# Performance work log

Hardware: AMD Instinct MI355X
Metric: run time of the kernel (lower is better)

The kernel has to match this reference:

```python
import jax, jax.numpy as jnp
import numpy as np
from jax import lax

P = 16        # patch spatial size (C = 3 * P * P = 768)
CH = 3        # channels per patch
H = 8         # num attention heads
EPS_BN = 1e-3 # keras BatchNormalization default epsilon
EPS_LN = 1e-3 # keras LayerNormalization default epsilon


def _layernorm(x, g, b):
    mu = jnp.mean(x, axis=-1, keepdims=True)
    var = jnp.mean(jnp.square(x - mu), axis=-1, keepdims=True)
    return (x - mu) * lax.rsqrt(var + EPS_LN) * g + b


def setup_inputs() -> dict:
    key = jax.random.key(0)
    ks = jax.random.split(key, 8)
    B, N, C, DFF = 8, 1024, 768, 3072
    s = 0.02
    return {
        "encoded_patches": jax.random.normal(ks[0], (B, N, C), jnp.float32),
        "qconv_w": jax.random.normal(ks[1], (3, 3, CH, CH), jnp.float32) * 0.2,
        "reatten_w": jax.random.normal(ks[2], (H, H), jnp.float32) * 0.3,
        "reatten_b": jnp.zeros((H,), jnp.float32),
        "bn_gamma": jnp.ones((H,), jnp.float32),
        "bn_beta": jnp.zeros((H,), jnp.float32),
        "proj_w": jax.random.normal(ks[3], (C, C), jnp.float32) * s,
        "proj_b": jnp.zeros((C,), jnp.float32),
        "ffn_w1": jax.random.normal(ks[4], (C, DFF), jnp.float32) * s,
        "ffn_b1": jnp.zeros((DFF,), jnp.float32),
        "ffn_w2": jax.random.normal(ks[5], (DFF, C), jnp.float32) * s,
        "ffn_b2": jnp.zeros((C,), jnp.float32),
        "ln1_g": jnp.ones((C,), jnp.float32),
        "ln1_b": jnp.zeros((C,), jnp.float32),
        "ln2_g": jnp.ones((C,), jnp.float32),
        "ln2_b": jnp.zeros((C,), jnp.float32),
    }


def reference(encoded_patches, qconv_w, reatten_w, reatten_b, bn_gamma, bn_beta,
              proj_w, proj_b, ffn_w1, ffn_b1, ffn_w2, ffn_b2,
              ln1_g, ln1_b, ln2_g, ln2_b):
    B, N, C = encoded_patches.shape
    hd = C // H
    scale = jnp.float32(hd) ** -0.5

    # create_queries: unflatten [B,N,C] -> [B*N,P,P,CH], 3x3 'same' conv,
    # flatten back and split heads -> [B,H,N,hd]. Source uses qconv2d for
    # q, k AND v, so q == k == v; compute once.
    y = encoded_patches.reshape(B * N, P, P, CH)
    y = lax.conv_general_dilated(y, qconv_w, (1, 1), 'SAME',
                                 dimension_numbers=('NHWC', 'HWIO', 'NHWC'))
    q = y.reshape(B, N, H, hd).transpose(0, 2, 1, 3)  # [B,H,N,hd]
    k = q
    v = q

    # attention scores + softmax: [B,H,N,N]
    attn = jax.nn.softmax(jnp.einsum('bhnd,bhmd->bhnm', q, k) * scale, axis=-1)

    # re-attention: 1x1 conv mixing heads + BatchNorm (inference: mean=0, var=1)
    attn = jnp.einsum('bhnm,gh->bgnm', attn, reatten_w) + reatten_b[None, :, None, None]
    bn_s = bn_gamma * lax.rsqrt(jnp.float32(1.0) + EPS_BN)
    attn = attn * bn_s[None, :, None, None] + bn_beta[None, :, None, None]
    # reatten_scale = 1.0 (transform_scale=False)

    x = jnp.einsum('bhnm,bhmd->bhnd', attn, v)        # [B,H,N,hd]
    x = x.transpose(0, 2, 1, 3).reshape(B, N, C)
    x = x @ proj_w + proj_b

    x = x + encoded_patches          # residual
    x = _layernorm(x, ln1_g, ln1_b)  # LN1

    h = jax.nn.gelu(x @ ffn_w1 + ffn_b1, approximate=False)
    x = (h @ ffn_w2 + ffn_b2) + x    # FFN + residual
    x = _layernorm(x, ln2_g, ln2_b)  # LN2
    return x
```

## Files before the change

### kernel.cpp

```cpp
#include <hip/hip_runtime.h>
#include <hip/hip_bf16.h>
#include <math.h>

#define B_ 8
#define N_ 1024
#define C_ 768
#define H_ 8
#define HD_ 96
#define DFF_ 3072
#define SC2_ 0.14724454f
#define SH2_ 11.5415602f

typedef __attribute__((ext_vector_type(8))) short bf16x8;
typedef __attribute__((ext_vector_type(4))) float f32x4;
typedef __attribute__((ext_vector_type(4))) short sh4;

__device__ __forceinline__ short f2bf(float f){
  __hip_bfloat16 h = __float2bfloat16(f);
  return __builtin_bit_cast(short, h);
}
__device__ __forceinline__ float bf2f(short s){
  unsigned u = ((unsigned)(unsigned short)s) << 16;
  return __builtin_bit_cast(float, u);
}
#define MFMA16(a,b,c) __builtin_amdgcn_mfma_f32_16x16x32_bf16((a),(b),(c),0,0,0)

__device__ __forceinline__ void gload16(const void* g, void* l){
  __builtin_amdgcn_global_load_lds((const __attribute__((address_space(1))) unsigned int*)g,
                                   (__attribute__((address_space(3))) unsigned int*)l, 16, 0, 0);
}

__global__ void conv_q_kernel(const float* __restrict__ x, const float* __restrict__ w,
                              short* __restrict__ qb){
  int p = blockIdx.x;
  int t = threadIdx.x;
  __shared__ float xs[768];
  __shared__ float ws[81];
  const float* xp = x + (size_t)p * 768;
  xs[t] = xp[t]; xs[t+256] = xp[t+256]; xs[t+512] = xp[t+512];
  if (t < 81) ws[t] = w[t];
  __syncthreads();
  int i = t >> 4, j = t & 15;
  float a0=0.f, a1=0.f, a2=0.f;
  #pragma unroll
  for (int di=0; di<3; ++di){
    int ii = i + di - 1;
    if (ii < 0 || ii > 15) continue;
    #pragma unroll
    for (int dj=0; dj<3; ++dj){
      int jj = j + dj - 1;
      if (jj < 0 || jj > 15) continue;
      const float* cell = &xs[(ii*16+jj)*3];
      const float* wp = &ws[(di*3+dj)*9];
      #pragma unroll
      for (int ci=0; ci<3; ++ci){
        float xv = cell[ci];
        a0 += xv * wp[ci*3+0];
        a1 += xv * wp[ci*3+1];
        a2 += xv * wp[ci*3+2];
      }
    }
  }
  short* qp = qb + (size_t)p*768 + t*3;
  qp[0]=f2bf(a0); qp[1]=f2bf(a1); qp[2]=f2bf(a2);
}

__global__ void vt_kernel(const short* __restrict__ in, short* __restrict__ out){
  __shared__ short tile[32][33];
  int b = blockIdx.z;
  int c0 = blockIdx.x*32, n0 = blockIdx.y*32;
  int t = threadIdx.x;
  const short* ib = in + (size_t)b*N_*C_;
  short* ob = out + (size_t)b*C_*N_;
  #pragma unroll
  for (int i=0;i<4;i++){
    int idx = i*256+t; int r = idx>>5, cc = idx&31;
    tile[r][cc] = ib[(size_t)(n0+r)*C_ + c0+cc];
  }
  __syncthreads();
  #pragma unroll
  for (int i=0;i<4;i++){
    int idx = i*256+t; int r = idx>>5, cc = idx&31;
    ob[(size_t)(c0+r)*N_ + n0+cc] = tile[cc][r];
  }
}

__global__ void wtrans_kernel(const float* __restrict__ in, short* __restrict__ out,
                              int K, int Nn){
  __shared__ float tile[32][33];
  int n0 = blockIdx.x*32, k0 = blockIdx.y*32;
  int t = threadIdx.x;
  #pragma unroll
  for (int i=0;i<4;i++){
    int idx=i*256+t; int r=idx>>5, cc=idx&31;
    tile[r][cc] = in[(size_t)(k0+r)*Nn + n0+cc];
  }
  __syncthreads();
  #pragma unroll
  for (int i=0;i<4;i++){
    int idx=i*256+t; int r=idx>>5, cc=idx&31;
    out[(size_t)(n0+r)*K + k0+cc] = f2bf(tile[cc][r]);
  }
}

__global__ __launch_bounds__(256, 2)
void qkexp_kernel(const short* __restrict__ qb, short* __restrict__ Pt,
                  float* __restrict__ lsums, int b0)
{
  __shared__ short Ks[64*104];
  int bid = blockIdx.x;
  int bhl = bid >> 4, nt = bid & 15;
  int b = b0 + (bhl >> 3), h = bhl & 7;
  int n0 = nt*64;
  int t = threadIdx.x, w = t>>6, l = t&63, lg = l>>4, lr = l&15;
  const short* qbase = qb + (size_t)b*N_*C_;

  bf16x8 qf[3];
  #pragma unroll
  for (int kc=0;kc<3;++kc)
    qf[kc] = *(const bf16x8*)(qbase + (size_t)(n0 + w*16 + lr)*C_ + h*HD_ + kc*32 + lg*8);

  bf16x8 kreg[3];
  #pragma unroll
  for (int i=0;i<3;++i){
    int id = i*256+t; int r = id/12, c = id%12;
    kreg[i] = *(const bf16x8*)(qbase + (size_t)r*C_ + h*HD_ + c*8);
  }

  float lsum = 0.f;
  short* prow = Pt + ((size_t)bhl*1024 + n0 + w*16 + lr)*1024;

  for (int mt=0; mt<16; ++mt){
    int m0 = mt*64;
    __syncthreads();
    #pragma unroll
    for (int i=0;i<3;++i){
      int id = i*256+t; int r = id/12, c = id%12;
      *(bf16x8*)&Ks[r*104 + c*8] = kreg[i];
    }
    __syncthreads();
    if (mt < 15){
      int m1 = m0 + 64;
      #pragma unroll
      for (int i=0;i<3;++i){
        int id = i*256+t; int r = id/12, c = id%12;
        kreg[i] = *(const bf16x8*)(qbase + (size_t)(m1+r)*C_ + h*HD_ + c*8);
      }
    }
    #pragma unroll
    for (int s=0;s<4;++s){
      f32x4 sacc = (f32x4){0.f,0.f,0.f,0.f};
      bf16x8 kf[3];
      #pragma unroll
      for (int kc=0;kc<3;++kc)
        kf[kc] = *(const bf16x8*)&Ks[(s*16+lr)*104 + kc*32 + lg*8];
      #pragma unroll
      for (int kc=0;kc<3;++kc)
        sacc = MFMA16(kf[kc], qf[kc], sacc);
      sh4 pv;
      #pragma unroll
      for (int r=0;r<4;++r){
        float e = exp2f(sacc[r]*SC2_ - SH2_);
        lsum += e;
        pv[r] = f2bf(e);
      }
      *(sh4*)&prow[m0 + s*16 + lg*4] = pv;
    }
  }
  lsum += __shfl_xor(lsum, 16);
  lsum += __shfl_xor(lsum, 32);
  if (l < 16) lsums[(size_t)bhl*1024 + n0 + w*16 + l] = lsum;
}

__device__ __forceinline__ void load_mix(const short* __restrict__ Pt, int b_local,
                                         int n0, int m0, int t,
                                         const float wl[4][8], float cw, bf16x8 amc[4]){
  #pragma unroll
  for (int i=0;i<4;++i){
    int r = i*32 + (t>>3), mo = t&7;
    const short* p0 = Pt + ((size_t)(b_local*8)*1024 + (size_t)(n0+r))*1024 + m0 + mo*8;
    float pm[8];
    #pragma unroll
    for (int j=0;j<8;++j) pm[j] = cw;
    #pragma unroll
    for (int h=0;h<8;++h){
      bf16x8 ph = *(const bf16x8*)(p0 + (size_t)h*1024*1024);
      #pragma unroll
      for (int j=0;j<8;++j) pm[j] += wl[i][h]*bf2f(ph[j]);
    }
    #pragma unroll
    for (int j=0;j<8;++j) amc[i][j] = f2bf(pm[j]);
  }
}

__global__ __launch_bounds__(256, 2)
void mixpv_kernel(const short* __restrict__ Pt, const float* __restrict__ lsums,
                  const short* __restrict__ vt, const float* __restrict__ rw,
                  const float* __restrict__ rb, const float* __restrict__ bng,
                  const float* __restrict__ bnb, short* __restrict__ out, int b0)
{
  __shared__ short Am[128*68];
  int bid = blockIdx.x;
  int rank = bid>>3;
  int g = rank & 7;
  int p = (bid&7) + ((rank>>3)<<3);
  int b_local = p>>3;
  int n0 = (p&7)*128;
  int b = b0 + b_local;
  int t = threadIdx.x, w = t>>6, l = t&63, lg = l>>4, lr = l&15;

  float bns = bng[g]*rsqrtf(1.001f);
  float cw = rb[g]*bns + bnb[g];
  float wl[4][8];
  #pragma unroll
  for (int i=0;i<4;++i){
    int r = i*32 + (t>>3);
    #pragma unroll
    for (int h=0;h<8;++h)
      wl[i][h] = (rw[g*8+h]*bns) / lsums[(size_t)(b_local*8+h)*1024 + n0 + r];
  }

  f32x4 acc[2][6];
  #pragma unroll
  for (int a=0;a<2;++a)
    #pragma unroll
    for (int nt=0;nt<6;++nt) acc[a][nt] = (f32x4){0.f,0.f,0.f,0.f};

  bf16x8 amc[4];
  load_mix(Pt, b_local, n0, 0, t, wl, cw, amc);
  const short* vbase = vt + (size_t)b*C_*N_ + (size_t)g*HD_*N_;

  for (int mt=0; mt<16; ++mt){
    int m0 = mt*64;
    __syncthreads();
    #pragma unroll
    for (int i=0;i<4;++i){
      int r = i*32 + (t>>3), mo = t&7;
      *(bf16x8*)&Am[r*68 + mo*8] = amc[i];
    }
    __syncthreads();
    if (mt < 15) load_mix(Pt, b_local, n0, m0+64, t, wl, cw, amc);
    #pragma unroll
    for (int kc=0;kc<2;++kc){
      bf16x8 af[2], bfr[6];
      #pragma unroll
      for (int a=0;a<2;++a)
        af[a] = *(const bf16x8*)&Am[(w*32 + a*16 + lr)*68 + kc*32 + lg*8];
      #pragma unroll
      for (int nt=0;nt<6;++nt)
        bfr[nt] = *(const bf16x8*)(vbase + (size_t)(nt*16+lr)*N_ + m0 + kc*32 + lg*8);
      #pragma unroll
      for (int a=0;a<2;++a)
        #pragma unroll
        for (int nt=0;nt<6;++nt)
          acc[a][nt] = MFMA16(af[a], bfr[nt], acc[a][nt]);
    }
  }

  short* obase = out + (size_t)b*N_*C_;
  #pragma unroll
  for (int a=0;a<2;++a)
    #pragma unroll
    for (int nt=0;nt<6;++nt)
      #pragma unroll
      for (int r=0;r<4;++r)
        obase[(size_t)(n0 + w*32 + a*16 + lg*4 + r)*C_ + g*HD_ + nt*16 + lr]
            = f2bf(acc[a][nt][r]);
}

template<int EPI>
__global__ __launch_bounds__(256, 3)
void gemm_bt_kernel(const short* __restrict__ A, const short* __restrict__ Bt,
                    const float* __restrict__ bias, const float* __restrict__ res,
                    float* __restrict__ Of, short* __restrict__ Ob,
                    int M, int Nn, int K)
{
  __shared__ short As[8192];
  __shared__ short Bs[8192];
  int gm = blockIdx.y*128, gn = blockIdx.x*128;
  int tid = threadIdx.x;
  int w = tid>>6, l = tid&63, lg = l>>4, lr = l&15;
  int wr = w>>1, wc = w&1;
  f32x4 acc[4][4];
  #pragma unroll
  for (int mt=0;mt<4;++mt)
    #pragma unroll
    for (int nt=0;nt<4;++nt) acc[mt][nt] = (f32x4){0.f,0.f,0.f,0.f};

  int srow = l>>3, scol = (l&7)*8;

  for (int kb=0; kb<K; kb+=64){
    __syncthreads();
    #pragma unroll
    for (int j=0;j<4;++j){
      int row = j*32 + w*8 + srow;
      gload16(A  + (size_t)(gm+row)*K + kb + scol, &As[j*2048 + w*512]);
      gload16(Bt + (size_t)(gn+row)*K + kb + scol, &Bs[j*2048 + w*512]);
    }
    __syncthreads();
    #pragma unroll
    for (int kc=0;kc<2;++kc){
      bf16x8 af[4], bfr[4];
      #pragma unroll
      for (int mt=0;mt<4;++mt)
        af[mt] = *(const bf16x8*)&As[(wr*64+mt*16+lr)*64 + kc*32 + lg*8];
      #pragma unroll
      for (int nt=0;nt<4;++nt)
        bfr[nt] = *(const bf16x8*)&Bs[(wc*64+nt*16+lr)*64 + kc*32 + lg*8];
      #pragma unroll
      for (int mt=0;mt<4;++mt)
        #pragma unroll
        for (int nt=0;nt<4;++nt)
          acc[mt][nt] = MFMA16(af[mt], bfr[nt], acc[mt][nt]);
    }
  }
  #pragma unroll
  for (int mt=0;mt<4;++mt){
    #pragma unroll
    for (int nt=0;nt<4;++nt){
      #pragma unroll
      for (int r=0;r<4;++r){
        int row = gm + wr*64 + mt*16 + lg*4 + r;
        int col = gn + wc*64 + nt*16 + lr;
        float v = acc[mt][nt][r] + bias[col];
        if (EPI == 0){
          v += res[(size_t)row*Nn + col];
          Of[(size_t)row*Nn + col] = v;
        } else {
          v = 0.5f*v*(1.0f + erff(v*0.70710678118654752f));
          Ob[(size_t)row*Nn + col] = f2bf(v);
        }
      }
    }
  }
}

template<int WB>
__global__ void ln_kernel(const float* __restrict__ in, const float* __restrict__ gam,
                          const float* __restrict__ bet, float* __restrict__ of,
                          short* __restrict__ ob)
{
  int row = blockIdx.x*4 + (threadIdx.x>>6);
  int l = threadIdx.x & 63;
  const float* ip = in + (size_t)row*C_;
  float v[12];
  #pragma unroll
  for (int i=0;i<3;i++) *(float4*)&v[i*4] = *(const float4*)(ip + i*256 + l*4);
  float s = 0.f;
  #pragma unroll
  for (int i=0;i<12;i++) s += v[i];
  #pragma unroll
  for (int off=1; off<64; off<<=1) s += __shfl_xor(s, off);
  float mu = s * (1.0f/768.0f);
  float q = 0.f;
  #pragma unroll
  for (int i=0;i<12;i++){ float d = v[i]-mu; q += d*d; }
  #pragma unroll
  for (int off=1; off<64; off<<=1) q += __shfl_xor(q, off);
  float rstd = rsqrtf(q*(1.0f/768.0f) + 1e-3f);
  #pragma unroll
  for (int i=0;i<3;i++){
    float4 gv = *(const float4*)(gam + i*256 + l*4);
    float4 bv = *(const float4*)(bet + i*256 + l*4);
    float o0 = (v[i*4+0]-mu)*rstd*gv.x + bv.x;
    float o1 = (v[i*4+1]-mu)*rstd*gv.y + bv.y;
    float o2 = (v[i*4+2]-mu)*rstd*gv.z + bv.z;
    float o3 = (v[i*4+3]-mu)*rstd*gv.w + bv.w;
    float4 ov = {o0,o1,o2,o3};
    *(float4*)(of + (size_t)row*C_ + i*256 + l*4) = ov;
    if (WB){
      sh4 obv = { f2bf(o0), f2bf(o1), f2bf(o2), f2bf(o3) };
      *(sh4*)(ob + (size_t)row*C_ + i*256 + l*4) = obv;
    }
  }
}

extern "C" void kernel_launch(void* const* d_in, const int* in_sizes, int n_in,
                              void* d_out, int out_size, void* d_ws, size_t ws_size,
                              hipStream_t stream)
{
  const float* enc       = (const float*)d_in[0];
  const float* qconv_w   = (const float*)d_in[1];
  const float* reatten_w = (const float*)d_in[2];
  const float* reatten_b = (const float*)d_in[3];
  const float* bn_gamma  = (const float*)d_in[4];
  const float* bn_beta   = (const float*)d_in[5];
  const float* proj_w    = (const float*)d_in[6];
  const float* proj_b    = (const float*)d_in[7];
  const float* ffn_w1    = (const float*)d_in[8];
  const float* ffn_b1    = (const float*)d_in[9];
  const float* ffn_w2    = (const float*)d_in[10];
  const float* ffn_b2    = (const float*)d_in[11];
  const float* ln1_g     = (const float*)d_in[12];
  const float* ln1_b     = (const float*)d_in[13];
  const float* ln2_g     = (const float*)d_in[14];
  const float* ln2_b     = (const float*)d_in[15];
  float* outp = (float*)d_out;

  char* ws = (char*)d_ws;
  short* qbuf  = (short*)(ws);
  short* vtbuf = (short*)(ws + 12582912);
  short* atbuf = (short*)(ws + 25165824);
  short* ptbuf = (short*)(ws + 37748736);
  float* lsums = (float*)(ws + 104857600);
  float* ypre  = (float*)(ws + 37748736);
  float* x1    = (float*)(ws + 62914560);
  short* x1b   = (short*)(ws + 88080384);
  short* hbuf  = (short*)(ws + 100663296);
  short* wpt   = (short*)(ws + 150994944);
  short* w1t   = (short*)(ws + 152174592);
  short* w2t   = (short*)(ws + 156893184);

  conv_q_kernel<<<B_*N_, 256, 0, stream>>>(enc, qconv_w, qbuf);
  vt_kernel<<<dim3(C_/32, N_/32, B_), 256, 0, stream>>>(qbuf, vtbuf);
  wtrans_kernel<<<dim3(C_/32,  C_/32), 256, 0, stream>>>(proj_w, wpt, C_,  C_);
  wtrans_kernel<<<dim3(DFF_/32, C_/32), 256, 0, stream>>>(ffn_w1, w1t, C_,  DFF_);
  wtrans_kernel<<<dim3(C_/32, DFF_/32), 256, 0, stream>>>(ffn_w2, w2t, DFF_, C_);

  for (int half=0; half<2; ++half){
    int b0 = half*4;
    qkexp_kernel<<<512, 256, 0, stream>>>(qbuf, ptbuf, lsums, b0);
    mixpv_kernel<<<256, 256, 0, stream>>>(ptbuf, lsums, vtbuf, reatten_w, reatten_b,
                                          bn_gamma, bn_beta, atbuf, b0);
  }

  gemm_bt_kernel<0><<<dim3(C_/128, (B_*N_)/128), 256, 0, stream>>>(
      atbuf, wpt, proj_b, enc, ypre, nullptr, B_*N_, C_, C_);
  ln_kernel<1><<<(B_*N_)/4, 256, 0, stream>>>(ypre, ln1_g, ln1_b, x1, x1b);
  gemm_bt_kernel<1><<<dim3(DFF_/128, (B_*N_)/128), 256, 0, stream>>>(
      x1b, w1t, ffn_b1, nullptr, nullptr, hbuf, B_*N_, DFF_, C_);
  gemm_bt_kernel<0><<<dim3(C_/128, (B_*N_)/128), 256, 0, stream>>>(
      hbuf, w2t, ffn_b2, x1, ypre, nullptr, B_*N_, C_, DFF_);
  ln_kernel<0><<<(B_*N_)/4, 256, 0, stream>>>(ypre, ln2_g, ln2_b, outp, nullptr);
}
```

Baseline: 404.0 us.

## Double-buffer GEMM LDS tiles with XOR swizzle and stage epilogue through LDS

The bf16 GEMM kernel now double-buffers its A/B tiles in a 64KB LDS region, so the next K-slab loads while MFMAs run on the current one. LDS reads and writes use an XOR swizzle to avoid bank conflicts. The epilogue writes accumulators to LDS and then does coalesced float4 reads of bias and residual and vectorized stores, instead of scattered scalar accesses. The larger LDS footprint lowers the occupancy target from 3 to 2 blocks per CU.

```diff
diff --git a/kernel.cpp b/kernel.cpp
--- a/kernel.cpp
+++ b/kernel.cpp
@@ -269,68 +269,113 @@
 }
 
 template<int EPI>
-__global__ __launch_bounds__(256, 3)
+__global__ __launch_bounds__(256, 2)
 void gemm_bt_kernel(const short* __restrict__ A, const short* __restrict__ Bt,
                     const float* __restrict__ bias, const float* __restrict__ res,
                     float* __restrict__ Of, short* __restrict__ Ob,
                     int M, int Nn, int K)
 {
-  __shared__ short As[8192];
-  __shared__ short Bs[8192];
+  __shared__ __align__(16) char smem[65536];
+  short* Sb = (short*)smem;
   int gm = blockIdx.y*128, gn = blockIdx.x*128;
   int tid = threadIdx.x;
   int w = tid>>6, l = tid&63, lg = l>>4, lr = l&15;
   int wr = w>>1, wc = w&1;
+  int srow = l>>3;
+  int sg = (l&7) ^ srow;
+
+  const short* Ap = A  + (size_t)(gm + w*8 + srow)*K + sg*8;
+  const short* Bp = Bt + (size_t)(gn + w*8 + srow)*K + sg*8;
+
   f32x4 acc[4][4];
   #pragma unroll
   for (int mt=0;mt<4;++mt)
     #pragma unroll
     for (int nt=0;nt<4;++nt) acc[mt][nt] = (f32x4){0.f,0.f,0.f,0.f};
 
-  int srow = l>>3, scol = (l&7)*8;
-
-  for (int kb=0; kb<K; kb+=64){
-    __syncthreads();
+  int nk = K >> 6;
+
+  {
+    short* dA = Sb; short* dB = Sb + 8192;
     #pragma unroll
     for (int j=0;j<4;++j){
-      int row = j*32 + w*8 + srow;
-      gload16(A  + (size_t)(gm+row)*K + kb + scol, &As[j*2048 + w*512]);
-      gload16(Bt + (size_t)(gn+row)*K + kb + scol, &Bs[j*2048 + w*512]);
-    }
-    __syncthreads();
+      gload16(Ap + (size_t)j*32*K, dA + (j*32 + w*8)*64);
+      gload16(Bp + (size_t)j*32*K, dB + (j*32 + w*8)*64);
+    }
+  }
+  asm volatile("s_waitcnt vmcnt(0)" ::: "memory");
+  __syncthreads();
+
+  int cur = 0;
+  for (int t=0; t<nk; ++t){
+    if (t+1 < nk){
+      short* dA = Sb + (cur^1)*16384;
+      short* dB = dA + 8192;
+      int kb = (t+1)<<6;
+      #pragma unroll
+      for (int j=0;j<4;++j){
+        gload16(Ap + (size_t)j*32*K + kb, dA + (j*32 + w*8)*64);
+        gload16(Bp + (size_t)j*32*K + kb, dB + (j*32 + w*8)*64);
+      }
+    }
+    short* CA = Sb + cur*16384;
+    short* CB = CA + 8192;
     #pragma unroll
     for (int kc=0;kc<2;++kc){
       bf16x8 af[4], bfr[4];
       #pragma unroll
-      for (int mt=0;mt<4;++mt)
-        af[mt] = *(const bf16x8*)&As[(wr*64+mt*16+lr)*64 + kc*32 + lg*8];
-      #pragma unroll
-      for (int nt=0;nt<4;++nt)
-        bfr[nt] = *(const bf16x8*)&Bs[(wc*64+nt*16+lr)*64 + kc*32 + lg*8];
+      for (int mt=0;mt<4;++mt){
+        int row = wr*64+mt*16+lr;
+        af[mt] = *(const bf16x8*)&CA[row*64 + (((kc*4+lg)^(lr&7))*8)];
+      }
+      #pragma unroll
+      for (int nt=0;nt<4;++nt){
+        int row = wc*64+nt*16+lr;
+        bfr[nt] = *(const bf16x8*)&CB[row*64 + (((kc*4+lg)^(lr&7))*8)];
+      }
       #pragma unroll
       for (int mt=0;mt<4;++mt)
         #pragma unroll
         for (int nt=0;nt<4;++nt)
           acc[mt][nt] = MFMA16(af[mt], bfr[nt], acc[mt][nt]);
     }
-  }
-  #pragma unroll
-  for (int mt=0;mt<4;++mt){
-    #pragma unroll
-    for (int nt=0;nt<4;++nt){
+    asm volatile("s_waitcnt vmcnt(0)" ::: "memory");
+    __syncthreads();
+    cur ^= 1;
+  }
+
+  float* Cl = (float*)smem;
+  #pragma unroll
+  for (int mt=0;mt<4;++mt)
+    #pragma unroll
+    for (int nt=0;nt<4;++nt)
       #pragma unroll
       for (int r=0;r<4;++r){
-        int row = gm + wr*64 + mt*16 + lg*4 + r;
-        int col = gn + wc*64 + nt*16 + lr;
-        float v = acc[mt][nt][r] + bias[col];
-        if (EPI == 0){
-          v += res[(size_t)row*Nn + col];
-          Of[(size_t)row*Nn + col] = v;
-        } else {
-          v = 0.5f*v*(1.0f + erff(v*0.70710678118654752f));
-          Ob[(size_t)row*Nn + col] = f2bf(v);
-        }
-      }
+        int row = wr*64 + mt*16 + lg*4 + r;
+        int col = wc*64 + nt*16 + lr;
+        Cl[row*128 + (col ^ ((row&7)<<2))] = acc[mt][nt][r];
+      }
+  __syncthreads();
+  #pragma unroll
+  for (int seg=0; seg<16; ++seg){
+    int row = seg*8 + (tid>>5);
+    int col = (tid&31)*4;
+    int colp = col ^ ((row&7)<<2);
+    f32x4 c = *(f32x4*)&Cl[row*128 + colp];
+    float4 bi = *(const float4*)&bias[gn+col];
+    size_t goff = (size_t)(gm+row)*Nn + gn + col;
+    if (EPI == 0){
+      float4 rs = *(const float4*)&res[goff];
+      float4 o = { c[0]+bi.x+rs.x, c[1]+bi.y+rs.y, c[2]+bi.z+rs.z, c[3]+bi.w+rs.w };
+      *(float4*)&Of[goff] = o;
+    } else {
+      float v0 = c[0]+bi.x, v1 = c[1]+bi.y, v2 = c[2]+bi.z, v3 = c[3]+bi.w;
+      v0 = 0.5f*v0*(1.0f + erff(v0*0.70710678118654752f));
+      v1 = 0.5f*v1*(1.0f + erff(v1*0.70710678118654752f));
+      v2 = 0.5f*v2*(1.0f + erff(v2*0.70710678118654752f));
+      v3 = 0.5f*v3*(1.0f + erff(v3*0.70710678118654752f));
+      sh4 ob = { f2bf(v0), f2bf(v1), f2bf(v2), f2bf(v3) };
+      *(sh4*)&Ob[goff] = ob;
     }
   }
 }
```

Result: faster. 387.0 us (-4.2%).
